# Kernel optimization log

Hardware: AMD Instinct MI355X
Metric: run time of the kernel (lower is better)

Reference implementation:

```python
import jax, jax.numpy as jnp
import numpy as np

B, C, H, W = 4, 64, 128, 128
Q = 65536
OUT_SIZE = 256  # output image side -> cell = 2/OUT_SIZE
HIDDEN = 256
D_IN = C + 2 + 2  # feat + rel_coord + rel_cell


def setup_inputs() -> dict:
    key = jax.random.key(0)
    ks = jax.random.split(key, 8)
    feat = jax.random.normal(ks[0], (B, C, H, W), dtype=jnp.float32)
    coord = jax.random.uniform(ks[1], (B, Q, 2), dtype=jnp.float32, minval=-1.0, maxval=1.0)
    cell = jnp.full((B, Q, 2), 2.0 / OUT_SIZE, dtype=jnp.float32)

    def lin(k, din, dout):
        return jax.random.normal(k, (din, dout), dtype=jnp.float32) * (1.0 / np.sqrt(din))

    w0 = lin(ks[2], D_IN, HIDDEN)
    w1 = lin(ks[3], HIDDEN, HIDDEN)
    w2 = lin(ks[4], HIDDEN, HIDDEN)
    w3 = lin(ks[5], HIDDEN, HIDDEN)
    w4 = lin(ks[6], HIDDEN, 3)
    z = lambda d: jnp.zeros((d,), dtype=jnp.float32)
    return {"feat": feat, "coord": coord, "cell": cell,
            "w0": w0, "b0": z(HIDDEN), "w1": w1, "b1": z(HIDDEN),
            "w2": w2, "b2": z(HIDDEN), "w3": w3, "b3": z(HIDDEN),
            "w4": w4, "b4": z(3)}


def _liif(feat, coord, cell, ws, bs):
    b, c, h, w = feat.shape
    eps = 1e-6
    rx, ry = 1.0 / h, 1.0 / w  # 2/h/2, 2/w/2
    # local ensemble shifts, loop order vx outer, vy inner: (-1,-1),(-1,1),(1,-1),(1,1)
    shifts = jnp.array([[-rx, -ry], [-rx, ry], [rx, -ry], [rx, ry]], dtype=feat.dtype) + eps
    feat_flat = feat.reshape(b, c, h * w)
    cell_scale = jnp.array([h, w], dtype=feat.dtype)
    rel_cell = cell * cell_scale  # same for all branches

    def branch(shift):
        cshift = jnp.clip(coord + shift, -1.0 + eps, 1.0 - eps)
        # nearest grid_sample, align_corners=False: idx = floor((x+1)*size/2), clamped
        iy = jnp.clip(jnp.floor((cshift[..., 0] + 1.0) * (h * 0.5)), 0.0, h - 1.0).astype(jnp.int32)
        ix = jnp.clip(jnp.floor((cshift[..., 1] + 1.0) * (w * 0.5)), 0.0, w - 1.0).astype(jnp.int32)
        idx = iy * w + ix  # [B, Q]
        q_feat = jnp.take_along_axis(feat_flat, idx[:, None, :], axis=2)  # [B, C, Q]
        q_feat = q_feat.transpose(0, 2, 1)  # [B, Q, C]
        # feat_coord at the gathered pixel (make_coord values)
        qc0 = -1.0 + (2.0 * iy.astype(feat.dtype) + 1.0) / h
        qc1 = -1.0 + (2.0 * ix.astype(feat.dtype) + 1.0) / w
        rel0 = (coord[..., 0] - qc0) * h
        rel1 = (coord[..., 1] - qc1) * w
        inp = jnp.concatenate([q_feat, rel0[..., None], rel1[..., None], rel_cell], axis=-1)
        x = inp
        for wi, bi in zip(ws[:-1], bs[:-1]):
            x = jax.nn.relu(x @ wi + bi)
        pred = x @ ws[-1] + bs[-1]  # [B, Q, 3]
        area = jnp.abs(rel0 * rel1) + 1e-9  # [B, Q]
        return pred, area

    preds, areas = jax.vmap(branch)(shifts)  # [4,B,Q,3], [4,B,Q]
    tot = areas.sum(axis=0)
    # diagonal weight swap: 0<->3, 1<->2  == reverse
    wgt = areas[::-1] / tot
    return (preds * wgt[..., None]).sum(axis=0)  # [B, Q, 3]


def reference(feat, coord, cell, w0, b0, w1, b1, w2, b2, w3, b3, w4, b4):
    ws = [w0, w1, w2, w3, w4]
    bs = [b0, b1, b2, b3, b4]
    return _liif(feat, coord, cell, ws, bs)
```

## Files before the change

kernel.cpp:

```cpp
#include <hip/hip_runtime.h>
#include <cstdint>

typedef __bf16 bf16x8 __attribute__((ext_vector_type(8)));
typedef float f32x4 __attribute__((ext_vector_type(4)));
typedef unsigned int u32x4 __attribute__((ext_vector_type(4)));
typedef unsigned int u32x2 __attribute__((ext_vector_type(2)));
typedef unsigned short u16;
typedef unsigned int u32;

#define HH 128
#define WW 128
#define CC 64
#define QQ 65536
#define BB 4

#define RS 264

#define L0_OFF 0
#define L1_OFF 24576
#define L2_OFF 90112
#define L3_OFF 155648
#define W4_OFF 221184
#define FEATT_BYTE_OFF 524288u

__global__ void pack_weights(const float* __restrict__ w0,
                             const float* __restrict__ w1,
                             const float* __restrict__ w2,
                             const float* __restrict__ w3,
                             const float* __restrict__ w4,
                             u16* __restrict__ ws_us) {
    int bid = blockIdx.x;
    int lane = threadIdx.x;
    int tile, nk, off, Ksrc, Ncols, NT;
    const float* w;
    if (bid < 48)       { tile = bid;       nk = 3; off = L0_OFF; w = w0; Ksrc = 68;  Ncols = 256; NT = 16; }
    else if (bid < 176) { tile = bid - 48;  nk = 8; off = L1_OFF; w = w1; Ksrc = 256; Ncols = 256; NT = 16; }
    else if (bid < 304) { tile = bid - 176; nk = 8; off = L2_OFF; w = w2; Ksrc = 256; Ncols = 256; NT = 16; }
    else if (bid < 432) { tile = bid - 304; nk = 8; off = L3_OFF; w = w3; Ksrc = 256; Ncols = 256; NT = 16; }
    else                { tile = bid - 432; nk = 8; off = W4_OFF; w = w4; Ksrc = 256; Ncols = 3;   NT = 1;  }
    int kt = tile % nk;
    int nt = tile / nk;
    int n = nt * 16 + (lane & 15);
    int kbase = kt * 32 + (lane >> 4) * 8;
    unsigned int d[4];
    for (int i = 0; i < 4; ++i) {
        unsigned int lo, hi;
        {
            int k = kbase + 2 * i;
            float x = (k < Ksrc && n < Ncols) ? w[k * Ncols + n] : 0.0f;
            __bf16 hb = (__bf16)x;
            lo = (unsigned int)__builtin_bit_cast(u16, hb);
        }
        {
            int k = kbase + 2 * i + 1;
            float x = (k < Ksrc && n < Ncols) ? w[k * Ncols + n] : 0.0f;
            __bf16 hb = (__bf16)x;
            hi = (unsigned int)__builtin_bit_cast(u16, hb);
        }
        d[i] = lo | (hi << 16);
    }
    u32x4 pk = { d[0], d[1], d[2], d[3] };
    int dst = off + (kt * NT + nt) * 512 + lane * 8;
    *reinterpret_cast<u32x4*>(ws_us + dst) = pk;
}

__global__ void prep_featT(const float* __restrict__ feat, u16* __restrict__ featT) {
    __shared__ u16 tile[128 * 66];
    int bid = blockIdx.x;
    int b = bid >> 7, y = bid & 127;
    for (int idx = threadIdx.x; idx < CC * WW; idx += 256) {
        int c = idx >> 7, x = idx & 127;
        float v = feat[(((b * CC + c) * HH + y) * WW) + x];
        __bf16 hb = (__bf16)v;
        tile[x * 66 + c] = __builtin_bit_cast(u16, hb);
    }
    __syncthreads();
    for (int idx = threadIdx.x; idx < 2048; idx += 256) {
        int x = idx >> 4, c4 = (idx & 15) * 4;
        const u16* src = tile + x * 66 + c4;
        u32x2 d;
        d[0] = (unsigned int)src[0] | ((unsigned int)src[1] << 16);
        d[1] = (unsigned int)src[2] | ((unsigned int)src[3] << 16);
        *reinterpret_cast<u32x2*>(featT + ((b * HH + y) * WW + x) * CC + c4) = d;
    }
}

__device__ __forceinline__ void preload_w(u32x4 wpre[4], const u32x4* __restrict__ wbase,
                                          int voff) {
#pragma unroll
    for (int fi = 0; fi < 4; ++fi)
        wpre[fi] = wbase[voff + fi * 64];
}

template <int NK>
__device__ __forceinline__ void gemm_layer(const u16* __restrict__ src,
                                           u16* __restrict__ dst,
                                           const u32x4* __restrict__ wbase,
                                           const float* __restrict__ bias,
                                           int wave, int lane,
                                           const u32x4 wpre[4]) {
    f32x4 acc[4][4] = {};
    const int l15 = lane & 15;
    const int qd = lane >> 4;
    const int voff = wave * 256 + lane;
    const u16* xb = src + l15 * RS + qd * 8;
    u16* db = dst + l15 * RS + wave * 64 + qd * 4;

    u32x4 wq[3][4];
#pragma unroll
    for (int fi = 0; fi < 4; ++fi) wq[0][fi] = wpre[fi];
    if (NK > 1) {
        const u32x4* wn = wbase + 1024;
#pragma unroll
        for (int fi = 0; fi < 4; ++fi) wq[1][fi] = wn[voff + fi * 64];
    }

    bf16x8 xc[4], xn[4];
#pragma unroll
    for (int st = 0; st < 4; ++st)
        xc[st] = __builtin_bit_cast(bf16x8,
            *reinterpret_cast<const u32x4*>(xb + st * 16 * RS));

#pragma unroll
    for (int kt = 0; kt < NK; ++kt) {
        if (kt + 2 < NK) {
            const u32x4* wn = wbase + (kt + 2) * 1024;
#pragma unroll
            for (int fi = 0; fi < 4; ++fi)
                wq[(kt + 2) % 3][fi] = wn[voff + fi * 64];
        }
        if (kt + 1 < NK) {
#pragma unroll
            for (int st = 0; st < 4; ++st)
                xn[st] = __builtin_bit_cast(bf16x8,
                    *reinterpret_cast<const u32x4*>(xb + st * 16 * RS + (kt + 1) * 32));
        }
#pragma unroll
        for (int fi = 0; fi < 4; ++fi) {
            bf16x8 wf = __builtin_bit_cast(bf16x8, wq[kt % 3][fi]);
#pragma unroll
            for (int st = 0; st < 4; ++st)
                acc[fi][st] = __builtin_amdgcn_mfma_f32_16x16x32_bf16(
                    wf, xc[st], acc[fi][st], 0, 0, 0);
        }
        if (kt + 1 < NK) {
#pragma unroll
            for (int st = 0; st < 4; ++st) xc[st] = xn[st];
        }
    }

#pragma unroll
    for (int fi = 0; fi < 4; ++fi) {
        int fbase = (wave * 4 + fi) * 16 + qd * 4;
        f32x4 bv = *reinterpret_cast<const f32x4*>(bias + fbase);
#pragma unroll
        for (int st = 0; st < 4; ++st) {
            float v0 = fmaxf(acc[fi][st][0] + bv[0], 0.0f);
            float v1 = fmaxf(acc[fi][st][1] + bv[1], 0.0f);
            float v2 = fmaxf(acc[fi][st][2] + bv[2], 0.0f);
            float v3 = fmaxf(acc[fi][st][3] + bv[3], 0.0f);
            __bf16 h0 = (__bf16)v0, h1 = (__bf16)v1, h2 = (__bf16)v2, h3 = (__bf16)v3;
            u32x2 d;
            d[0] = (u32)__builtin_bit_cast(u16, h0) | ((u32)__builtin_bit_cast(u16, h1) << 16);
            d[1] = (u32)__builtin_bit_cast(u16, h2) | ((u32)__builtin_bit_cast(u16, h3) << 16);
            *reinterpret_cast<u32x2*>(db + st * 16 * RS + fi * 16) = d;
        }
    }
}

__global__ __launch_bounds__(256, 2) void liif_main(
    const float* __restrict__ coord, const float* __restrict__ cell,
    const float* __restrict__ b0, const float* __restrict__ b1,
    const float* __restrict__ b2, const float* __restrict__ b3,
    const float* __restrict__ b4,
    const u16* __restrict__ wpack, const u16* __restrict__ featT,
    float* __restrict__ out) {
    __shared__ u16 bufA[64 * RS];
    __shared__ u16 bufB[64 * RS];
    __shared__ float areasLDS[64];

    const int t = threadIdx.x;
    const int wave = t >> 6, lane = t & 63;
    const int row = t >> 2, p = t & 3;

    const int bq = blockIdx.x * 16 + (row >> 2);
    const int v = row & 3;
    const int b = bq >> 16;
    const float c0 = coord[bq * 2 + 0];
    const float c1 = coord[bq * 2 + 1];
    const float rc0 = cell[bq * 2 + 0] * 128.0f;
    const float rc1 = cell[bq * 2 + 1] * 128.0f;
    const float eps = 1e-6f;
    const float sx = ((v & 2) ? 0.0078125f : -0.0078125f) + eps;
    const float sy = ((v & 1) ? 0.0078125f : -0.0078125f) + eps;
    float cs0 = fminf(fmaxf(c0 + sx, -1.0f + eps), 1.0f - eps);
    float cs1 = fminf(fmaxf(c1 + sy, -1.0f + eps), 1.0f - eps);
    float fy = fminf(fmaxf(floorf((cs0 + 1.0f) * 64.0f), 0.0f), 127.0f);
    float fx = fminf(fmaxf(floorf((cs1 + 1.0f) * 64.0f), 0.0f), 127.0f);
    int iy = (int)fy, ix = (int)fx;
    float qc0 = -1.0f + (2.0f * fy + 1.0f) * 0.0078125f;
    float qc1 = -1.0f + (2.0f * fx + 1.0f) * 0.0078125f;
    float rel0 = (c0 - qc0) * 128.0f;
    float rel1 = (c1 - qc1) * 128.0f;
    float area = fabsf(rel0 * rel1) + 1e-9f;

    {
        const u16* fr = featT + (((b * HH + iy) * WW + ix) * CC) + p * 16;
        u32x4 f0 = *reinterpret_cast<const u32x4*>(fr);
        u32x4 f1 = *reinterpret_cast<const u32x4*>(fr + 8);
        u16* sb = bufA + row * RS;
        *reinterpret_cast<u32x4*>(sb + p * 16) = f0;
        *reinterpret_cast<u32x4*>(sb + p * 16 + 8) = f1;
        u32x4 e = { 0u, 0u, 0u, 0u };
        if (p == 0) {
            __bf16 h0 = (__bf16)rel0, h1 = (__bf16)rel1, h2 = (__bf16)rc0, h3 = (__bf16)rc1;
            e[0] = (u32)__builtin_bit_cast(u16, h0) | ((u32)__builtin_bit_cast(u16, h1) << 16);
            e[1] = (u32)__builtin_bit_cast(u16, h2) | ((u32)__builtin_bit_cast(u16, h3) << 16);
            areasLDS[row] = area;
        }
        *reinterpret_cast<u32x4*>(sb + 64 + p * 8) = e;
    }

    const u32x4* wp = reinterpret_cast<const u32x4*>(wpack);
    const u32x4* wp0 = wp + (L0_OFF / 8);
    const u32x4* wp1 = wp + (L1_OFF / 8);
    const u32x4* wp2 = wp + (L2_OFF / 8);
    const u32x4* wp3 = wp + (L3_OFF / 8);
    const u32x4* wp4 = wp + (W4_OFF / 8);
    const int voff = wave * 256 + lane;

    u32x4 wpre[4];
    preload_w(wpre, wp0, voff);
    __syncthreads();
    gemm_layer<3>(bufA, bufB, wp0, b0, wave, lane, wpre);
    preload_w(wpre, wp1, voff);
    __syncthreads();
    gemm_layer<8>(bufB, bufA, wp1, b1, wave, lane, wpre);
    preload_w(wpre, wp2, voff);
    __syncthreads();
    gemm_layer<8>(bufA, bufB, wp2, b2, wave, lane, wpre);
    preload_w(wpre, wp3, voff);
    __syncthreads();
    gemm_layer<8>(bufB, bufA, wp3, b3, wave, lane, wpre);

    u32x4 w4f[8];
#pragma unroll
    for (int kt = 0; kt < 8; ++kt) w4f[kt] = wp4[kt * 64 + lane];
    __syncthreads();

    const int l15 = lane & 15;
    const int qd = lane >> 4;
    const u16* xb = bufA + (wave * 16 + l15) * RS + qd * 8;
    f32x4 accf = {};
#pragma unroll
    for (int kt = 0; kt < 8; ++kt) {
        bf16x8 x = __builtin_bit_cast(bf16x8,
            *reinterpret_cast<const u32x4*>(xb + kt * 32));
        accf = __builtin_amdgcn_mfma_f32_16x16x32_bf16(
            __builtin_bit_cast(bf16x8, w4f[kt]), x, accf, 0, 0, 0);
    }
    float a = areasLDS[wave * 16 + l15];
    float a1 = a + __shfl_xor(a, 1);
    float asum = a1 + __shfl_xor(a1, 2);
    float aopp = __shfl_xor(a, 3);
    float wgt = aopp / asum;
    float o0 = (accf[0] + b4[0]) * wgt;
    float o1 = (accf[1] + b4[1]) * wgt;
    float o2 = (accf[2] + b4[2]) * wgt;
    o0 += __shfl_xor(o0, 1); o0 += __shfl_xor(o0, 2);
    o1 += __shfl_xor(o1, 1); o1 += __shfl_xor(o1, 2);
    o2 += __shfl_xor(o2, 1); o2 += __shfl_xor(o2, 2);

    if (qd == 0 && (l15 & 3) == 0) {
        int obq = blockIdx.x * 16 + wave * 4 + (l15 >> 2);
        out[obq * 3 + 0] = o0;
        out[obq * 3 + 1] = o1;
        out[obq * 3 + 2] = o2;
    }
}

extern "C" void kernel_launch(void* const* d_in, const int* in_sizes, int n_in,
                              void* d_out, int out_size, void* d_ws, size_t ws_size,
                              hipStream_t stream) {
    const float* feat  = (const float*)d_in[0];
    const float* coord = (const float*)d_in[1];
    const float* cell  = (const float*)d_in[2];
    const float* w0 = (const float*)d_in[3];
    const float* b0 = (const float*)d_in[4];
    const float* w1 = (const float*)d_in[5];
    const float* b1 = (const float*)d_in[6];
    const float* w2 = (const float*)d_in[7];
    const float* b2 = (const float*)d_in[8];
    const float* w3 = (const float*)d_in[9];
    const float* b3 = (const float*)d_in[10];
    const float* w4 = (const float*)d_in[11];
    const float* b4 = (const float*)d_in[12];

    u16* ws_us = (u16*)d_ws;
    u16* featT = (u16*)((char*)d_ws + FEATT_BYTE_OFF);

    hipLaunchKernelGGL(pack_weights, dim3(440), dim3(64), 0, stream,
                       w0, w1, w2, w3, w4, ws_us);
    hipLaunchKernelGGL(prep_featT, dim3(BB * HH), dim3(256), 0, stream, feat, featT);
    hipLaunchKernelGGL(liif_main, dim3((BB * QQ) / 16), dim3(256), 0, stream,
                       coord, cell, b0, b1, b2, b3, b4, ws_us, featT,
                       (float*)d_out);
}
```

Before: 559.4 us.

## Use single in-place LDS activation buffer and raise occupancy to four blocks

Replaces the ping-pong pair of shared activation buffers with one buffer updated in place, adding a barrier inside each layer between the last operand read and the epilogue write. Halving LDS per block lets launch bounds ask for four blocks per CU instead of two, so more waves can hide memory and MFMA latency. The next layer's first weight fragments are now prefetched before that barrier, overlapping the global load with the sync. Risks are extra barriers per layer and tighter register limits at the higher occupancy, which could cause spills in the unrolled GEMM.

```diff
diff --git a/kernel.cpp b/kernel.cpp
--- a/kernel.cpp
+++ b/kernel.cpp
@@ -93,18 +93,20 @@
 }
 
 template <int NK>
-__device__ __forceinline__ void gemm_layer(const u16* __restrict__ src,
-                                           u16* __restrict__ dst,
+__device__ __forceinline__ void gemm_layer(u16* buf,
                                            const u32x4* __restrict__ wbase,
                                            const float* __restrict__ bias,
                                            int wave, int lane,
-                                           const u32x4 wpre[4]) {
+                                           const u32x4 wpre[4],
+                                           u32x4 wnxt[4],
+                                           const u32x4* __restrict__ wnb,
+                                           int vnxt) {
     f32x4 acc[4][4] = {};
     const int l15 = lane & 15;
     const int qd = lane >> 4;
     const int voff = wave * 256 + lane;
-    const u16* xb = src + l15 * RS + qd * 8;
-    u16* db = dst + l15 * RS + wave * 64 + qd * 4;
+    const u16* xb = buf + l15 * RS + qd * 8;
+    u16* db = buf + l15 * RS + wave * 64 + qd * 4;
 
     u32x4 wq[3][4];
 #pragma unroll
@@ -148,6 +150,11 @@
             for (int st = 0; st < 4; ++st) xc[st] = xn[st];
         }
     }
+
+#pragma unroll
+    for (int fi = 0; fi < 4; ++fi) wnxt[fi] = wnb[vnxt + fi * 64];
+
+    __syncthreads();
 
 #pragma unroll
     for (int fi = 0; fi < 4; ++fi) {
@@ -168,7 +175,7 @@
     }
 }
 
-__global__ __launch_bounds__(256, 2) void liif_main(
+__global__ __launch_bounds__(256, 4) void liif_main(
     const float* __restrict__ coord, const float* __restrict__ cell,
     const float* __restrict__ b0, const float* __restrict__ b1,
     const float* __restrict__ b2, const float* __restrict__ b3,
@@ -176,7 +183,6 @@
     const u16* __restrict__ wpack, const u16* __restrict__ featT,
     float* __restrict__ out) {
     __shared__ u16 bufA[64 * RS];
-    __shared__ u16 bufB[64 * RS];
     __shared__ float areasLDS[64];
 
     const int t = threadIdx.x;
@@ -229,23 +235,19 @@
     const u32x4* wp4 = wp + (W4_OFF / 8);
     const int voff = wave * 256 + lane;
 
-    u32x4 wpre[4];
-    preload_w(wpre, wp0, voff);
-    __syncthreads();
-    gemm_layer<3>(bufA, bufB, wp0, b0, wave, lane, wpre);
-    preload_w(wpre, wp1, voff);
-    __syncthreads();
-    gemm_layer<8>(bufB, bufA, wp1, b1, wave, lane, wpre);
-    preload_w(wpre, wp2, voff);
-    __syncthreads();
-    gemm_layer<8>(bufA, bufB, wp2, b2, wave, lane, wpre);
-    preload_w(wpre, wp3, voff);
-    __syncthreads();
-    gemm_layer<8>(bufB, bufA, wp3, b3, wave, lane, wpre);
-
-    u32x4 w4f[8];
-#pragma unroll
-    for (int kt = 0; kt < 8; ++kt) w4f[kt] = wp4[kt * 64 + lane];
+    u32x4 wA[4], wB[4];
+    preload_w(wA, wp0, voff);
+    __syncthreads();
+    gemm_layer<3>(bufA, wp0, b0, wave, lane, wA, wB, wp1, voff);
+    __syncthreads();
+    gemm_layer<8>(bufA, wp1, b1, wave, lane, wB, wA, wp2, voff);
+    __syncthreads();
+    gemm_layer<8>(bufA, wp2, b2, wave, lane, wA, wB, wp3, voff);
+    __syncthreads();
+    gemm_layer<8>(bufA, wp3, b3, wave, lane, wB, wA, wp4, lane);
+    u32x4 w4hi[4];
+#pragma unroll
+    for (int kt = 0; kt < 4; ++kt) w4hi[kt] = wp4[(kt + 4) * 64 + lane];
     __syncthreads();
 
     const int l15 = lane & 15;
@@ -253,11 +255,18 @@
     const u16* xb = bufA + (wave * 16 + l15) * RS + qd * 8;
     f32x4 accf = {};
 #pragma unroll
-    for (int kt = 0; kt < 8; ++kt) {
+    for (int kt = 0; kt < 4; ++kt) {
         bf16x8 x = __builtin_bit_cast(bf16x8,
             *reinterpret_cast<const u32x4*>(xb + kt * 32));
         accf = __builtin_amdgcn_mfma_f32_16x16x32_bf16(
-            __builtin_bit_cast(bf16x8, w4f[kt]), x, accf, 0, 0, 0);
+            __builtin_bit_cast(bf16x8, wA[kt]), x, accf, 0, 0, 0);
+    }
+#pragma unroll
+    for (int kt = 4; kt < 8; ++kt) {
+        bf16x8 x = __builtin_bit_cast(bf16x8,
+            *reinterpret_cast<const u32x4*>(xb + kt * 32));
+        accf = __builtin_amdgcn_mfma_f32_16x16x32_bf16(
+            __builtin_bit_cast(bf16x8, w4hi[kt - 4]), x, accf, 0, 0, 0);
     }
     float a = areasLDS[wave * 16 + l15];
     float a1 = a + __shfl_xor(a, 1);
```

After: 525.8 us. 1.06x faster.
